# Kernel optimization log

Measured on AMD Instinct MI355X. Metric: run time of the kernel, lower is better.

## Reference

```python
import jax, jax.numpy as jnp
import numpy as np

HEAD = 8
EMB = 512
D_K = EMB // HEAD


def setup_inputs() -> dict:
    key = jax.random.key(0)
    ks = jax.random.split(key, 12)
    B, S = 2, 2048
    scale = 1.0 / np.sqrt(EMB)
    inp = {
        "query": jax.random.normal(ks[0], (B, S, EMB), jnp.float32),
        "key": jax.random.normal(ks[1], (B, S, EMB), jnp.float32),
        "value": jax.random.normal(ks[2], (B, S, EMB), jnp.float32),
        # subsequentMask(size): lower-triangular causal mask, shape [1, S, S]
        "mask": jnp.tril(jnp.ones((1, S, S), jnp.int32)),
        "Wq": jax.random.normal(ks[3], (EMB, EMB), jnp.float32) * scale,
        "bq": jnp.zeros((EMB,), jnp.float32),
        "Wk": jax.random.normal(ks[4], (EMB, EMB), jnp.float32) * scale,
        "bk": jnp.zeros((EMB,), jnp.float32),
        "Wv": jax.random.normal(ks[5], (EMB, EMB), jnp.float32) * scale,
        "bv": jnp.zeros((EMB,), jnp.float32),
        "Wo": jax.random.normal(ks[6], (EMB, EMB), jnp.float32) * scale,
        "bo": jnp.zeros((EMB,), jnp.float32),
    }
    return inp


def _split_heads(x, B):
    # [B, S, E] -> [B, H, S, d_k]
    return x.reshape(B, -1, HEAD, D_K).transpose(0, 2, 1, 3)


def reference(query, key, value, mask, Wq, bq, Wk, bk, Wv, bv, Wo, bo):
    B, S, _ = query.shape
    # linear projections (x @ W^T + b, torch nn.Linear convention)
    q = _split_heads(query @ Wq.T + bq, B)
    k = _split_heads(key @ Wk.T + bk, B)
    v = _split_heads(value @ Wv.T + bv, B)
    # scaled dot-product attention; scores [B, H, S, S]
    scores = jnp.einsum('bhqd,bhkd->bhqk', q, k) / jnp.sqrt(jnp.float32(D_K))
    # mask [1,S,S] -> unsqueeze(0) -> [1,1,S,S]; masked_fill(mask==0, -1e9)
    m = mask[None, ...]  # [1, 1, S, S]
    scores = jnp.where(m == 0, jnp.float32(-1e9), scores)
    p_attn = jax.nn.softmax(scores, axis=-1)
    # dropout is identity at inference (deterministic reference)
    x = jnp.einsum('bhqk,bhkd->bhqd', p_attn, v)
    x = x.transpose(0, 2, 1, 3).reshape(B, S, EMB)
    return x @ Wo.T + bo
```

## Files before the change

### kernel.cpp

```cpp
#include <hip/hip_runtime.h>
#include <hip/hip_bf16.h>


#define SEQ 2048
#define EMB 512
#define NH  8
#define DKD 64

typedef __bf16 bf16x8 __attribute__((ext_vector_type(8)));
typedef float  f32x4  __attribute__((ext_vector_type(4)));
typedef _Float16 f16x8 __attribute__((ext_vector_type(8)));

__device__ __forceinline__ ushort f2bf(float f) {
  unsigned x = __float_as_uint(f);
  return (ushort)((x + 0x7fffu + ((x >> 16) & 1u)) >> 16);
}
__device__ __forceinline__ unsigned pkbf(float a, float b) {
  __hip_bfloat162 h = __float22bfloat162_rn(make_float2(a, b));
  unsigned u;
  __builtin_memcpy(&u, &h, 4);
  return u;
}

__device__ __forceinline__ void cp16(const ushort* g, ushort* l) {
  __builtin_amdgcn_global_load_lds(
      (const __attribute__((address_space(1))) void*)g,
      (__attribute__((address_space(3))) void*)l, 16, 0, 0);
}

__global__ __launch_bounds__(256) void cvt7(
    const float* s0, const float* s1, const float* s2, const float* s3,
    const float* s4, const float* s5, const float* s6,
    ushort* d0, ushort* d1, ushort* d2, ushort* d3,
    ushort* d4, ushort* d5, ushort* d6) {
  const float* src; ushort* dst; int n;
  switch (blockIdx.y) {
    case 0: src = s0; dst = d0; n = 2 * SEQ * EMB; break;
    case 1: src = s1; dst = d1; n = 2 * SEQ * EMB; break;
    case 2: src = s2; dst = d2; n = 2 * SEQ * EMB; break;
    case 3: src = s3; dst = d3; n = EMB * EMB;     break;
    case 4: src = s4; dst = d4; n = EMB * EMB;     break;
    case 5: src = s5; dst = d5; n = EMB * EMB;     break;
    default: src = s6; dst = d6; n = EMB * EMB;    break;
  }
  int i = (blockIdx.x * 256 + threadIdx.x) * 8;
  if (i >= n) return;
  float4 a = *reinterpret_cast<const float4*>(src + i);
  float4 b = *reinterpret_cast<const float4*>(src + i + 4);
  uint4 t = make_uint4(pkbf(a.x, a.y), pkbf(a.z, a.w),
                       pkbf(b.x, b.y), pkbf(b.z, b.w));
  *reinterpret_cast<uint4*>(dst + i) = t;
}

__device__ __forceinline__ void gemm_body(const ushort* __restrict__ X,
                                          const ushort* __restrict__ W,
                                          const float* __restrict__ bias,
                                          void* __restrict__ C,
                                          int wg, int mode, bool of32,
                                          float oscale,
                                          ushort* sA, ushort* sB) {
  const int N = EMB, K = EMB;
  const int tid = threadIdx.x;
  const int w = tid >> 6, lane = tid & 63, r16 = lane & 15, g = lane >> 4;
  const int nT = N / 64;
  const int m0 = (wg / nT) * 128;
  const int n0 = (wg % nT) * 64;
  const int wm = w * 32;

  f32x4 acc[2][4] = {};

  auto stage = [&](int buf, int k0) {
#pragma unroll
    for (int i = 0; i < 2; ++i) {
      const int s = i * 256 + w * 64 + lane;
      const int row = s >> 2;
      const int col = (s & 3) ^ ((row >> 1) & 3);
      cp16(X + (size_t)(m0 + row) * K + k0 + col * 8, sA + buf * 4096 + s * 8);
    }
    {
      const int s = w * 64 + lane;
      const int row = s >> 2;
      const int col = (s & 3) ^ ((row >> 1) & 3);
      cp16(W + (size_t)(n0 + row) * K + k0 + col * 8, sB + buf * 2048 + s * 8);
    }
  };

  stage(0, 0);
  const int NIT = K / 32;
  for (int it = 0; it < NIT; ++it) {
    const int cur = it & 1;
    __syncthreads();
    if (it + 1 < NIT) stage(cur ^ 1, (it + 1) * 32);

    const ushort* bA = sA + cur * 4096;
    const ushort* bB = sB + cur * 2048;
    bf16x8 af[2], bfr[4];
#pragma unroll
    for (int f = 0; f < 2; ++f) {
      const int row = wm + f * 16 + r16;
      af[f] = *reinterpret_cast<const bf16x8*>(bA + row * 32 + ((g ^ ((row >> 1) & 3)) << 3));
    }
#pragma unroll
    for (int t = 0; t < 4; ++t) {
      const int row = t * 16 + r16;
      bfr[t] = *reinterpret_cast<const bf16x8*>(bB + row * 32 + ((g ^ ((row >> 1) & 3)) << 3));
    }
#pragma unroll
    for (int f = 0; f < 2; ++f)
#pragma unroll
      for (int t = 0; t < 4; ++t)
        acc[f][t] = __builtin_amdgcn_mfma_f32_16x16x32_bf16(af[f], bfr[t], acc[f][t], 0, 0, 0);
  }

#pragma unroll
  for (int t = 0; t < 4; ++t) {
    const int n = n0 + t * 16 + r16;
    const float bv = bias[n];
#pragma unroll
    for (int f = 0; f < 2; ++f) {
#pragma unroll
      for (int r = 0; r < 4; ++r) {
        const int m = m0 + wm + f * 16 + g * 4 + r;
        const float v = (acc[f][t][r] + bv) * oscale;
        size_t addr;
        if (mode == 0) {
          addr = (size_t)m * N + n;
        } else {
          const int b = m >> 11, s = m & (SEQ - 1);
          const int h = n >> 6, dk = n & (DKD - 1);
          addr = (mode == 1) ? (((size_t)(b * NH + h) * SEQ + s) * DKD + dk)
                             : (((size_t)(b * NH + h) * DKD + dk) * SEQ + s);
        }
        if (of32) ((float*)C)[addr] = v;
        else      ((ushort*)C)[addr] = f2bf(v);
      }
    }
  }
}

__global__ __launch_bounds__(256) void proj_qkv(
    const ushort* Xq, const ushort* Xk, const ushort* Xv,
    const ushort* Wq, const ushort* Wk, const ushort* Wv,
    const float* bq, const float* bk, const float* bv,
    ushort* Qo, ushort* Ko, ushort* Vo) {
  __shared__ __align__(16) ushort sA[2 * 128 * 32];
  __shared__ __align__(16) ushort sB[2 * 64 * 32];
  const int z = blockIdx.z;
  const ushort* X = (z == 0) ? Xq : (z == 1) ? Xk : Xv;
  const ushort* W = (z == 0) ? Wq : (z == 1) ? Wk : Wv;
  const float* bias = (z == 0) ? bq : (z == 1) ? bk : bv;
  ushort* C = (z == 0) ? Qo : (z == 1) ? Ko : Vo;
  const int h = blockIdx.x;
  const int wg = (h & 7) * 32 + (h >> 3);
  gemm_body(X, W, bias, C, wg, (z == 2) ? 2 : 1, false,
            (z == 0) ? 0.18033688011112042f : 1.0f, sA, sB);
}

__global__ __launch_bounds__(256) void out_proj(const ushort* X, const ushort* W,
                                                const float* bias, float* C) {
  __shared__ __align__(16) ushort sA[2 * 128 * 32];
  __shared__ __align__(16) ushort sB[2 * 64 * 32];
  const int h = blockIdx.x;
  const int wg = (h & 7) * 32 + (h >> 3);
  gemm_body(X, W, bias, C, wg, 0, true, 1.0f, sA, sB);
}

__global__ __launch_bounds__(256) void flash_attn(
    const ushort* __restrict__ Q, const ushort* __restrict__ Kb,
    const ushort* __restrict__ Vt,
    _Float16* __restrict__ O0, _Float16* __restrict__ O1,
    _Float16* __restrict__ O2, _Float16* __restrict__ O3,
    _Float16* __restrict__ O4,
    float* __restrict__ P0, float* __restrict__ P1, float* __restrict__ P2,
    float* __restrict__ P3, float* __restrict__ P4) {
  __shared__ __align__(16) ushort sK[64 * 64];
  __shared__ __align__(16) ushort sV[64 * 64];
  __shared__ __align__(16) ushort sP[4][16 * 64];

  const int tid = threadIdx.x, w = tid >> 6, lane = tid & 63;
  const int r16 = lane & 15, g = lane >> 4;
  const int hwid = blockIdx.x;
  const int xcd = hwid & 7;
  const int i   = hwid >> 3;
  const int bh  = xcd * 2 + (i & 1);
  int rem = i >> 1;
  int qb = 31;
  int ns;
  for (;; --qb) {
    ns = (qb + 7) / 7;
    if (rem < ns) break;
    rem -= ns;
  }
  const int slot = rem;
  const int tiles = qb + 1;
  const int kt0 = (tiles * slot) / ns;
  const int kt1 = (tiles * (slot + 1)) / ns;

  const int q0 = qb * 64 + w * 16;
  const int q  = q0 + r16;

  const ushort* qp = Q + ((size_t)bh * SEQ + q0 + r16) * DKD + g * 8;
  const bf16x8 qf0 = *reinterpret_cast<const bf16x8*>(qp);
  const bf16x8 qf1 = *reinterpret_cast<const bf16x8*>(qp + 32);

  f32x4 oacc[4] = {};
  float psum = 0.f;

  const ushort* kbase = Kb + (size_t)bh * SEQ * DKD;
  const ushort* vbase = Vt + (size_t)bh * DKD * SEQ;

  auto stageKV = [&](int kb) {
#pragma unroll
    for (int ii = 0; ii < 2; ++ii) {
      const int s = ii * 256 + w * 64 + lane;
      const int row = s >> 3;
      const int col = (s & 7) ^ (row & 7);
      cp16(kbase + (size_t)(kb + row) * DKD + col * 8, &sK[(size_t)(ii * 256 + w * 64) * 8]);
      cp16(vbase + (size_t)row * SEQ + kb + col * 8,   &sV[(size_t)(ii * 256 + w * 64) * 8]);
    }
  };

  for (int kt = kt0; kt < kt1; ++kt) {
    const int kb = kt * 64;
    __syncthreads();
    stageKV(kb);
    __syncthreads();

    f32x4 sc[4] = {};
#pragma unroll
    for (int t = 0; t < 4; ++t) {
      const int row = t * 16 + r16;
      const bf16x8 a0 = *reinterpret_cast<const bf16x8*>(&sK[row * 64 + (((0 + g) ^ (row & 7)) << 3)]);
      const bf16x8 a1 = *reinterpret_cast<const bf16x8*>(&sK[row * 64 + (((4 + g) ^ (row & 7)) << 3)]);
      sc[t] = __builtin_amdgcn_mfma_f32_16x16x32_bf16(a0, qf0, sc[t], 0, 0, 0);
      sc[t] = __builtin_amdgcn_mfma_f32_16x16x32_bf16(a1, qf1, sc[t], 0, 0, 0);
    }

    const bool diag = (kb + 63) > q0;
    float p[16];
#pragma unroll
    for (int t = 0; t < 4; ++t)
#pragma unroll
      for (int r = 0; r < 4; ++r) {
        float e = __builtin_amdgcn_exp2f(sc[t][r]);
        if (diag && (kb + t * 16 + g * 4 + r) > q) e = 0.f;
        p[t * 4 + r] = e;
      }
    float s0 = (p[0] + p[1]) + (p[2] + p[3]);
    float s1 = (p[4] + p[5]) + (p[6] + p[7]);
    float s2 = (p[8] + p[9]) + (p[10] + p[11]);
    float s3 = (p[12] + p[13]) + (p[14] + p[15]);
    psum += (s0 + s1) + (s2 + s3);

#pragma unroll
    for (int t = 0; t < 4; ++t) {
      const unsigned lo = pkbf(p[t * 4],     p[t * 4 + 1]);
      const unsigned hi = pkbf(p[t * 4 + 2], p[t * 4 + 3]);
      const int key0 = t * 16 + g * 4;
      const int slt = (key0 >> 3) ^ (r16 & 7);
      *reinterpret_cast<uint2*>(&sP[w][r16 * 64 + slt * 8 + (key0 & 7)]) = make_uint2(lo, hi);
    }
    __asm__ volatile("s_waitcnt lgkmcnt(0)" ::: "memory");

    const bf16x8 pf0 = *reinterpret_cast<const bf16x8*>(&sP[w][r16 * 64 + (((0 + g) ^ (r16 & 7)) << 3)]);
    const bf16x8 pf1 = *reinterpret_cast<const bf16x8*>(&sP[w][r16 * 64 + (((4 + g) ^ (r16 & 7)) << 3)]);
#pragma unroll
    for (int t = 0; t < 4; ++t) {
      const int row = t * 16 + r16;
      const bf16x8 b0 = *reinterpret_cast<const bf16x8*>(&sV[row * 64 + (((0 + g) ^ (row & 7)) << 3)]);
      const bf16x8 b1 = *reinterpret_cast<const bf16x8*>(&sV[row * 64 + (((4 + g) ^ (row & 7)) << 3)]);
      oacc[t] = __builtin_amdgcn_mfma_f32_16x16x32_bf16(pf0, b0, oacc[t], 0, 0, 0);
      oacc[t] = __builtin_amdgcn_mfma_f32_16x16x32_bf16(pf1, b1, oacc[t], 0, 0, 0);
    }
  }

  psum += __shfl_xor(psum, 16);
  psum += __shfl_xor(psum, 32);
  float* Pc = (slot == 0) ? P0 : (slot == 1) ? P1 : (slot == 2) ? P2
            : (slot == 3) ? P3 : P4;
  _Float16* Oc = (slot == 0) ? O0 : (slot == 1) ? O1 : (slot == 2) ? O2
               : (slot == 3) ? O3 : O4;
  if (g == 0) Pc[(size_t)bh * SEQ + q0 + r16] = psum;
#pragma unroll
  for (int r = 0; r < 4; ++r) {
    const int mq = q0 + g * 4 + r;
#pragma unroll
    for (int t = 0; t < 4; ++t)
      Oc[((size_t)bh * SEQ + mq) * DKD + t * 16 + r16] = (_Float16)oacc[t][r];
  }
}

__global__ __launch_bounds__(256) void attn_norm(
    const _Float16* __restrict__ O0, const _Float16* __restrict__ O1,
    const _Float16* __restrict__ O2, const _Float16* __restrict__ O3,
    const _Float16* __restrict__ O4,
    const float* __restrict__ P0, const float* __restrict__ P1,
    const float* __restrict__ P2, const float* __restrict__ P3,
    const float* __restrict__ P4, ushort* __restrict__ Ab) {
  const int idx = blockIdx.x * 256 + threadIdx.x;
  const int d0 = (idx & 7) * 8;
  const int s  = (idx >> 3) & (SEQ - 1);
  const int bh = idx >> 14;
  const int qb = s >> 6;
  const int ns = (qb + 7) / 7;
  const size_t o = ((size_t)bh * SEQ + s) * DKD + d0;
  const size_t ps = (size_t)bh * SEQ + s;
  float r[8];
  {
    const f16x8 a = *reinterpret_cast<const f16x8*>(O0 + o);
#pragma unroll
    for (int k = 0; k < 8; ++k) r[k] = (float)a[k];
  }
  float pden = P0[ps];
  if (ns > 1) {
    const f16x8 a = *reinterpret_cast<const f16x8*>(O1 + o);
#pragma unroll
    for (int k = 0; k < 8; ++k) r[k] += (float)a[k];
    pden += P1[ps];
  }
  if (ns > 2) {
    const f16x8 a = *reinterpret_cast<const f16x8*>(O2 + o);
#pragma unroll
    for (int k = 0; k < 8; ++k) r[k] += (float)a[k];
    pden += P2[ps];
  }
  if (ns > 3) {
    const f16x8 a = *reinterpret_cast<const f16x8*>(O3 + o);
#pragma unroll
    for (int k = 0; k < 8; ++k) r[k] += (float)a[k];
    pden += P3[ps];
  }
  if (ns > 4) {
    const f16x8 a = *reinterpret_cast<const f16x8*>(O4 + o);
#pragma unroll
    for (int k = 0; k < 8; ++k) r[k] += (float)a[k];
    pden += P4[ps];
  }
  const float inv = 1.0f / pden;
#pragma unroll
  for (int k = 0; k < 8; ++k) r[k] *= inv;
  uint4 t = make_uint4(pkbf(r[0], r[1]), pkbf(r[2], r[3]),
                       pkbf(r[4], r[5]), pkbf(r[6], r[7]));
  const int bb = bh >> 3, hh = bh & 7;
  *reinterpret_cast<uint4*>(Ab + ((size_t)bb * SEQ + s) * EMB + hh * DKD + d0) = t;
}

extern "C" void kernel_launch(void* const* d_in, const int* in_sizes, int n_in,
                              void* d_out, int out_size, void* d_ws, size_t ws_size,
                              hipStream_t stream) {
  const float* q_in = (const float*)d_in[0];
  const float* k_in = (const float*)d_in[1];
  const float* v_in = (const float*)d_in[2];
  const float* Wq = (const float*)d_in[4];
  const float* bq = (const float*)d_in[5];
  const float* Wk = (const float*)d_in[6];
  const float* bk = (const float*)d_in[7];
  const float* Wv = (const float*)d_in[8];
  const float* bv = (const float*)d_in[9];
  const float* Wo = (const float*)d_in[10];
  const float* bo = (const float*)d_in[11];
  float* out = (float*)d_out;
  ushort* ws = (ushort*)d_ws;

  const size_t NX = (size_t)2 * SEQ * EMB;
  const size_t NW = (size_t)EMB * EMB;
  const size_t NO = (size_t)2 * NH * SEQ * DKD;
  ushort* Xq = ws;
  ushort* Xk = Xq + NX;
  ushort* Xv = Xk + NX;
  ushort* WqB = Xv + NX;
  ushort* WkB = WqB + NW;
  ushort* WvB = WkB + NW;
  ushort* WoB = WvB + NW;
  ushort* Qb  = WoB + NW;
  ushort* Kbf = Qb + NX;
  ushort* Vbf = Kbf + NX;
  ushort* Ab  = Vbf + NX;
  _Float16* O0 = (_Float16*)(Ab + NX);
  _Float16* O1 = O0 + NO;
  _Float16* O2 = O1 + NO;
  _Float16* O3 = O2 + NO;
  _Float16* O4 = O3 + NO;
  float*  P0  = (float*)(O4 + NO);
  float*  P1  = P0 + (size_t)2 * NH * SEQ;
  float*  P2  = P1 + (size_t)2 * NH * SEQ;
  float*  P3  = P2 + (size_t)2 * NH * SEQ;
  float*  P4  = P3 + (size_t)2 * NH * SEQ;

  dim3 blk(256);
  cvt7<<<dim3(1024, 7), blk, 0, stream>>>(q_in, k_in, v_in, Wq, Wk, Wv, Wo,
                                          Xq, Xk, Xv, WqB, WkB, WvB, WoB);
  proj_qkv<<<dim3((2 * SEQ / 128) * (EMB / 64), 1, 3), blk, 0, stream>>>(
      Xq, Xk, Xv, WqB, WkB, WvB, bq, bk, bv, Qb, Kbf, Vbf);
  flash_attn<<<dim3(1440), blk, 0, stream>>>(Qb, Kbf, Vbf,
                                             O0, O1, O2, O3, O4,
                                             P0, P1, P2, P3, P4);
  attn_norm<<<dim3(1024), blk, 0, stream>>>(O0, O1, O2, O3, O4,
                                            P0, P1, P2, P3, P4, Ab);
  out_proj<<<dim3((2 * SEQ / 128) * (EMB / 64)), blk, 0, stream>>>(Ab, WoB, bo, out);
}
```

Measured before the change: 157.4 us.

## Double-buffer K/V tiles in flash attention and reduce key-split count

Stages the next K/V tile into a second shared-memory buffer while the current tile is computed, replacing the two full barriers per iteration with a vmcnt wait plus barrier. It also changes the split-K partition from chunks of 7 tiles to 11, cutting the grid from 1440 to 1008 blocks and the partial output buffers from five to three. This reduces the partial-sum traffic in the normalization kernel. The trade-off is doubled LDS use per block, which may lower occupancy, and longer per-block work with less parallelism.

```diff
diff --git a/kernel.cpp b/kernel.cpp
--- a/kernel.cpp
+++ b/kernel.cpp
@@ -169,12 +169,10 @@
     const ushort* __restrict__ Q, const ushort* __restrict__ Kb,
     const ushort* __restrict__ Vt,
     _Float16* __restrict__ O0, _Float16* __restrict__ O1,
-    _Float16* __restrict__ O2, _Float16* __restrict__ O3,
-    _Float16* __restrict__ O4,
-    float* __restrict__ P0, float* __restrict__ P1, float* __restrict__ P2,
-    float* __restrict__ P3, float* __restrict__ P4) {
-  __shared__ __align__(16) ushort sK[64 * 64];
-  __shared__ __align__(16) ushort sV[64 * 64];
+    _Float16* __restrict__ O2,
+    float* __restrict__ P0, float* __restrict__ P1, float* __restrict__ P2) {
+  __shared__ __align__(16) ushort sK[2][64 * 64];
+  __shared__ __align__(16) ushort sV[2][64 * 64];
   __shared__ __align__(16) ushort sP[4][16 * 64];
 
   const int tid = threadIdx.x, w = tid >> 6, lane = tid & 63;
@@ -187,7 +185,7 @@
   int qb = 31;
   int ns;
   for (;; --qb) {
-    ns = (qb + 7) / 7;
+    ns = (qb + 11) / 11;
     if (rem < ns) break;
     rem -= ns;
   }
@@ -209,29 +207,40 @@
   const ushort* kbase = Kb + (size_t)bh * SEQ * DKD;
   const ushort* vbase = Vt + (size_t)bh * DKD * SEQ;
 
-  auto stageKV = [&](int kb) {
+  auto stageKV = [&](int kb, int buf) {
 #pragma unroll
     for (int ii = 0; ii < 2; ++ii) {
       const int s = ii * 256 + w * 64 + lane;
       const int row = s >> 3;
       const int col = (s & 7) ^ (row & 7);
-      cp16(kbase + (size_t)(kb + row) * DKD + col * 8, &sK[(size_t)(ii * 256 + w * 64) * 8]);
-      cp16(vbase + (size_t)row * SEQ + kb + col * 8,   &sV[(size_t)(ii * 256 + w * 64) * 8]);
+      cp16(kbase + (size_t)(kb + row) * DKD + col * 8, &sK[buf][(size_t)(ii * 256 + w * 64) * 8]);
+      cp16(vbase + (size_t)row * SEQ + kb + col * 8,   &sV[buf][(size_t)(ii * 256 + w * 64) * 8]);
     }
   };
 
+  stageKV(kt0 * 64, 0);
   for (int kt = kt0; kt < kt1; ++kt) {
+    const int cur = (kt - kt0) & 1;
     const int kb = kt * 64;
-    __syncthreads();
-    stageKV(kb);
-    __syncthreads();
+
+    if (kt + 1 < kt1) {
+      stageKV((kt + 1) * 64, cur ^ 1);
+      __asm__ volatile("s_waitcnt vmcnt(4)" ::: "memory");
+    } else {
+      __asm__ volatile("s_waitcnt vmcnt(0)" ::: "memory");
+    }
+    __builtin_amdgcn_sched_barrier(0);
+    __builtin_amdgcn_s_barrier();
+
+    const ushort* cK = sK[cur];
+    const ushort* cV = sV[cur];
 
     f32x4 sc[4] = {};
 #pragma unroll
     for (int t = 0; t < 4; ++t) {
       const int row = t * 16 + r16;
-      const bf16x8 a0 = *reinterpret_cast<const bf16x8*>(&sK[row * 64 + (((0 + g) ^ (row & 7)) << 3)]);
-      const bf16x8 a1 = *reinterpret_cast<const bf16x8*>(&sK[row * 64 + (((4 + g) ^ (row & 7)) << 3)]);
+      const bf16x8 a0 = *reinterpret_cast<const bf16x8*>(&cK[row * 64 + (((0 + g) ^ (row & 7)) << 3)]);
+      const bf16x8 a1 = *reinterpret_cast<const bf16x8*>(&cK[row * 64 + (((4 + g) ^ (row & 7)) << 3)]);
       sc[t] = __builtin_amdgcn_mfma_f32_16x16x32_bf16(a0, qf0, sc[t], 0, 0, 0);
       sc[t] = __builtin_amdgcn_mfma_f32_16x16x32_bf16(a1, qf1, sc[t], 0, 0, 0);
     }
@@ -267,19 +276,21 @@
 #pragma unroll
     for (int t = 0; t < 4; ++t) {
       const int row = t * 16 + r16;
-      const bf16x8 b0 = *reinterpret_cast<const bf16x8*>(&sV[row * 64 + (((0 + g) ^ (row & 7)) << 3)]);
-      const bf16x8 b1 = *reinterpret_cast<const bf16x8*>(&sV[row * 64 + (((4 + g) ^ (row & 7)) << 3)]);
+      const bf16x8 b0 = *reinterpret_cast<const bf16x8*>(&cV[row * 64 + (((0 + g) ^ (row & 7)) << 3)]);
+      const bf16x8 b1 = *reinterpret_cast<const bf16x8*>(&cV[row * 64 + (((4 + g) ^ (row & 7)) << 3)]);
       oacc[t] = __builtin_amdgcn_mfma_f32_16x16x32_bf16(pf0, b0, oacc[t], 0, 0, 0);
       oacc[t] = __builtin_amdgcn_mfma_f32_16x16x32_bf16(pf1, b1, oacc[t], 0, 0, 0);
     }
+
+    __asm__ volatile("s_waitcnt lgkmcnt(0)" ::: "memory");
+    __builtin_amdgcn_sched_barrier(0);
+    __builtin_amdgcn_s_barrier();
   }
 
   psum += __shfl_xor(psum, 16);
   psum += __shfl_xor(psum, 32);
-  float* Pc = (slot == 0) ? P0 : (slot == 1) ? P1 : (slot == 2) ? P2
-            : (slot == 3) ? P3 : P4;
-  _Float16* Oc = (slot == 0) ? O0 : (slot == 1) ? O1 : (slot == 2) ? O2
-               : (slot == 3) ? O3 : O4;
+  float* Pc = (slot == 0) ? P0 : (slot == 1) ? P1 : P2;
+  _Float16* Oc = (slot == 0) ? O0 : (slot == 1) ? O1 : O2;
   if (g == 0) Pc[(size_t)bh * SEQ + q0 + r16] = psum;
 #pragma unroll
   for (int r = 0; r < 4; ++r) {
@@ -292,17 +303,15 @@
 
 __global__ __launch_bounds__(256) void attn_norm(
     const _Float16* __restrict__ O0, const _Float16* __restrict__ O1,
-    const _Float16* __restrict__ O2, const _Float16* __restrict__ O3,
-    const _Float16* __restrict__ O4,
+    const _Float16* __restrict__ O2,
     const float* __restrict__ P0, const float* __restrict__ P1,
-    const float* __restrict__ P2, const float* __restrict__ P3,
-    const float* __restrict__ P4, ushort* __restrict__ Ab) {
+    const float* __restrict__ P2, ushort* __restrict__ Ab) {
   const int idx = blockIdx.x * 256 + threadIdx.x;
   const int d0 = (idx & 7) * 8;
   const int s  = (idx >> 3) & (SEQ - 1);
   const int bh = idx >> 14;
   const int qb = s >> 6;
-  const int ns = (qb + 7) / 7;
+  const int ns = (qb + 11) / 11;
   const size_t o = ((size_t)bh * SEQ + s) * DKD + d0;
   const size_t ps = (size_t)bh * SEQ + s;
   float r[8];
@@ -323,18 +332,6 @@
 #pragma unroll
     for (int k = 0; k < 8; ++k) r[k] += (float)a[k];
     pden += P2[ps];
-  }
-  if (ns > 3) {
-    const f16x8 a = *reinterpret_cast<const f16x8*>(O3 + o);
-#pragma unroll
-    for (int k = 0; k < 8; ++k) r[k] += (float)a[k];
-    pden += P3[ps];
-  }
-  if (ns > 4) {
-    const f16x8 a = *reinterpret_cast<const f16x8*>(O4 + o);
-#pragma unroll
-    for (int k = 0; k < 8; ++k) r[k] += (float)a[k];
-    pden += P4[ps];
   }
   const float inv = 1.0f / pden;
 #pragma unroll
@@ -379,23 +376,16 @@
   _Float16* O0 = (_Float16*)(Ab + NX);
   _Float16* O1 = O0 + NO;
   _Float16* O2 = O1 + NO;
-  _Float16* O3 = O2 + NO;
-  _Float16* O4 = O3 + NO;
-  float*  P0  = (float*)(O4 + NO);
+  float*  P0  = (float*)(O2 + NO);
   float*  P1  = P0 + (size_t)2 * NH * SEQ;
   float*  P2  = P1 + (size_t)2 * NH * SEQ;
-  float*  P3  = P2 + (size_t)2 * NH * SEQ;
-  float*  P4  = P3 + (size_t)2 * NH * SEQ;
 
   dim3 blk(256);
   cvt7<<<dim3(1024, 7), blk, 0, stream>>>(q_in, k_in, v_in, Wq, Wk, Wv, Wo,
                                           Xq, Xk, Xv, WqB, WkB, WvB, WoB);
   proj_qkv<<<dim3((2 * SEQ / 128) * (EMB / 64), 1, 3), blk, 0, stream>>>(
       Xq, Xk, Xv, WqB, WkB, WvB, bq, bk, bv, Qb, Kbf, Vbf);
-  flash_attn<<<dim3(1440), blk, 0, stream>>>(Qb, Kbf, Vbf,
-                                             O0, O1, O2, O3, O4,
-                                             P0, P1, P2, P3, P4);
-  attn_norm<<<dim3(1024), blk, 0, stream>>>(O0, O1, O2, O3, O4,
-                                            P0, P1, P2, P3, P4, Ab);
+  flash_attn<<<dim3(1008), blk, 0, stream>>>(Qb, Kbf, Vbf, O0, O1, O2, P0, P1, P2);
+  attn_norm<<<dim3(1024), blk, 0, stream>>>(O0, O1, O2, P0, P1, P2, Ab);
   out_proj<<<dim3((2 * SEQ / 128) * (EMB / 64)), blk, 0, stream>>>(Ab, WoB, bo, out);
 }
```

Result: no change. 156.3 us (-0.7%).
